# Kernel tuning notes

Hardware: AMD Instinct MI355X
Metric: run time of the kernel (lower is better)

The kernel has to match this reference:

```python
import jax, jax.numpy as jnp
import numpy as np

D = 64
H = 4
HD = D // H
N_MOL, E_MOL = 2048, 32768
N_PROT, E_PROT = 8192, 262144
LN_EPS = 1e-5


def _lin_params(key, d_in, d_out):
    k1, k2 = jax.random.split(key)
    lim = 1.0 / np.sqrt(d_in)
    w = jax.random.uniform(k1, (d_in, d_out), minval=-lim, maxval=lim, dtype=jnp.float32)
    b = jax.random.uniform(k2, (d_out,), minval=-lim, maxval=lim, dtype=jnp.float32)
    return w, b


def setup_inputs() -> dict:
    key = jax.random.key(0)
    ks = jax.random.split(key, 20)
    inp = {
        'x_mol': jax.random.normal(ks[0], (N_MOL, D), dtype=jnp.float32),
        'edge_index_mol': jax.random.randint(ks[1], (2, E_MOL), 0, N_MOL),
        'edge_attr_mol': jax.random.normal(ks[2], (E_MOL, D), dtype=jnp.float32),
        'x_prot': jax.random.normal(ks[3], (N_PROT, D), dtype=jnp.float32),
        'edge_index_prot': jax.random.randint(ks[4], (2, E_PROT), 0, N_PROT),
        'edge_attr_prot': jax.random.normal(ks[5], (E_PROT, D), dtype=jnp.float32),
    }
    # GINE MLPs: Linear -> ReLU -> Linear
    inp['mol_w1'], inp['mol_b1'] = _lin_params(ks[6], D, D)
    inp['mol_w2'], inp['mol_b2'] = _lin_params(ks[7], D, D)
    inp['prot_w1'], inp['prot_b1'] = _lin_params(ks[8], D, D)
    inp['prot_w2'], inp['prot_b2'] = _lin_params(ks[9], D, D)
    # cross-attn mol->prot (query=mol, key/value=prot)
    inp['mp_wq'], inp['mp_bq'] = _lin_params(ks[10], D, D)
    inp['mp_wk'], inp['mp_bk'] = _lin_params(ks[11], D, D)
    inp['mp_wv'], inp['mp_bv'] = _lin_params(ks[12], D, D)
    # cross-attn prot->mol (query=prot, key/value=mol)
    inp['pm_wq'], inp['pm_bq'] = _lin_params(ks[13], D, D)
    inp['pm_wk'], inp['pm_bk'] = _lin_params(ks[14], D, D)
    inp['pm_wv'], inp['pm_bv'] = _lin_params(ks[15], D, D)
    # layer norms
    inp['ln_mol_g'] = jnp.ones((D,), jnp.float32)
    inp['ln_mol_b'] = jnp.zeros((D,), jnp.float32)
    inp['ln_prot_g'] = jnp.ones((D,), jnp.float32)
    inp['ln_prot_b'] = jnp.zeros((D,), jnp.float32)
    return inp


def _gine_conv(x, edge_index, edge_attr, w1, b1, w2, b2, n_nodes):
    # message: relu(x_j + edge_attr); aggregate: mean at target; update: MLP((1+eps)*x + aggr), eps=0
    src, dst = edge_index[0], edge_index[1]
    msg = jax.nn.relu(x[src] + edge_attr)                       # [E, D]
    ssum = jax.ops.segment_sum(msg, dst, num_segments=n_nodes)  # [N, D]
    cnt = jax.ops.segment_sum(jnp.ones((msg.shape[0],), msg.dtype), dst, num_segments=n_nodes)
    aggr = ssum / jnp.maximum(cnt, 1.0)[:, None]
    h = x + aggr
    h = jax.nn.relu(h @ w1 + b1) @ w2 + b2
    return h


def _cross_attn(q_nodes, k_nodes, wq, bq, wk, bk, wv, bv):
    Nq, Nk = q_nodes.shape[0], k_nodes.shape[0]
    Q = (q_nodes @ wq + bq).reshape(Nq, H, HD)
    K = (k_nodes @ wk + bk).reshape(Nk, H, HD)
    V = (k_nodes @ wv + bv).reshape(Nk, H, HD)
    scores = jnp.einsum('qhd,khd->hqk', Q, K) / np.sqrt(HD).astype(np.float32)
    attn = jax.nn.softmax(scores, axis=-1)                      # [H, Nq, Nk]
    out = jnp.einsum('hqk,khd->qhd', attn, V).reshape(Nq, D)
    return out


def _layer_norm(x, g, b):
    mu = jnp.mean(x, axis=-1, keepdims=True)
    var = jnp.mean(jnp.square(x - mu), axis=-1, keepdims=True)
    return (x - mu) * jax.lax.rsqrt(var + LN_EPS) * g + b


def reference(x_mol, edge_index_mol, edge_attr_mol, x_prot, edge_index_prot, edge_attr_prot,
              mol_w1, mol_b1, mol_w2, mol_b2, prot_w1, prot_b1, prot_w2, prot_b2,
              mp_wq, mp_bq, mp_wk, mp_bk, mp_wv, mp_bv,
              pm_wq, pm_bq, pm_wk, pm_bk, pm_wv, pm_bv,
              ln_mol_g, ln_mol_b, ln_prot_g, ln_prot_b):
    h_mol = jax.nn.relu(_gine_conv(x_mol, edge_index_mol, edge_attr_mol,
                                   mol_w1, mol_b1, mol_w2, mol_b2, x_mol.shape[0]))
    h_prot = jax.nn.relu(_gine_conv(x_prot, edge_index_prot, edge_attr_prot,
                                    prot_w1, prot_b1, prot_w2, prot_b2, x_prot.shape[0]))
    h_mol_attn = _cross_attn(h_mol, h_prot, mp_wq, mp_bq, mp_wk, mp_bk, mp_wv, mp_bv)
    h_prot_attn = _cross_attn(h_prot, h_mol, pm_wq, pm_bq, pm_wk, pm_bk, pm_wv, pm_bv)
    out_mol = _layer_norm(h_mol + h_mol_attn, ln_mol_g, ln_mol_b)
    out_prot = _layer_norm(h_prot + h_prot_attn, ln_prot_g, ln_prot_b)
    return out_mol, out_prot
```

## Files before the change

kernel.cpp:

```cpp
#include <hip/hip_runtime.h>

#define NM 2048
#define EM 32768
#define NP 8192
#define EP 262144

typedef __attribute__((ext_vector_type(8))) short short8;
typedef __attribute__((ext_vector_type(4))) float f32x4;

#define LOG2E 1.44269504088896340736f

__device__ __forceinline__ float e2(float x) { return __builtin_amdgcn_exp2f(x); }
__device__ __forceinline__ unsigned int pk_bf16_tr(float a, float b) {
    return __builtin_amdgcn_perm(__float_as_uint(a), __float_as_uint(b), 0x03020706u);
}
__device__ __forceinline__ unsigned short cvt_bf16(float f) {
    unsigned int u = __float_as_uint(f);
    u = (u + 0x7fff + ((u >> 16) & 1)) >> 16;
    return (unsigned short)u;
}

__global__ __launch_bounds__(256) void hist_kernel(
    const int* __restrict__ ei_m, const int* __restrict__ ei_p,
    int* __restrict__ cnt_m, int* __restrict__ cnt_p)
{
    int idx = blockIdx.x * 256 + threadIdx.x;
    if (idx < EM) atomicAdd(&cnt_m[ei_m[EM + idx]], 1);
    int j = idx - EM;
    if (j >= 0 && j < EP) atomicAdd(&cnt_p[ei_p[EP + j]], 1);
}

__global__ __launch_bounds__(256) void scan_kernel(
    const int* __restrict__ cnt_m, const int* __restrict__ cnt_p,
    int* __restrict__ start_m, int* __restrict__ start_p,
    int* __restrict__ cur_m, int* __restrict__ cur_p)
{
    const int* cnt; int* start; int* cur; int n;
    if (blockIdx.x == 0) { cnt = cnt_m; start = start_m; cur = cur_m; n = NM; }
    else                 { cnt = cnt_p; start = start_p; cur = cur_p; n = NP; }
    int per = n >> 8;
    int tid = threadIdx.x;
    int base = tid * per;
    int s = 0;
    for (int i = 0; i < per; i++) s += cnt[base + i];
    __shared__ int wsum[4];
    int lane = tid & 63, w = tid >> 6;
    int v = s;
    #pragma unroll
    for (int off = 1; off < 64; off <<= 1) {
        int u = __shfl_up(v, off, 64);
        if (lane >= off) v += u;
    }
    if (lane == 63) wsum[w] = v;
    __syncthreads();
    int wo = 0;
    for (int i = 0; i < w; i++) wo += wsum[i];
    int run = wo + v - s;
    for (int i = 0; i < per; i++) {
        start[base + i] = run; cur[base + i] = run;
        run += cnt[base + i];
    }
    if (tid == 255) start[n] = run;
}

__global__ __launch_bounds__(256) void scatter_kernel(
    const int* __restrict__ ei_m, const int* __restrict__ ei_p,
    int* __restrict__ cur_m, int* __restrict__ cur_p,
    int* __restrict__ pidx_m, int* __restrict__ pidx_p)
{
    int idx = blockIdx.x * 256 + threadIdx.x;
    if (idx < EM) {
        int d = ei_m[EM + idx];
        int pos = atomicAdd(&cur_m[d], 1);
        pidx_m[pos] = (idx << 11) | ei_m[idx];
    }
    int j = idx - EM;
    if (j >= 0 && j < EP) {
        int d = ei_p[EP + j];
        int pos = atomicAdd(&cur_p[d], 1);
        pidx_p[pos] = (j << 13) | ei_p[j];
    }
}

__global__ __launch_bounds__(256) void node_aggr_kernel(
    const float* __restrict__ x_m, const float* __restrict__ ea_m,
    const int* __restrict__ start_m, const int* __restrict__ pidx_m,
    const float* __restrict__ x_p, const float* __restrict__ ea_p,
    const int* __restrict__ start_p, const int* __restrict__ pidx_p,
    float* __restrict__ h0_m, float* __restrict__ h0_p)
{
    int wave = threadIdx.x >> 6, lane = threadIdx.x & 63;
    int nid = blockIdx.x * 4 + wave;
    const float *x, *ea; const int *start, *pidx; float* h0; int n, sh, msk;
    if (nid < NM) { x = x_m; ea = ea_m; start = start_m; pidx = pidx_m; h0 = h0_m; n = nid; sh = 11; msk = 2047; }
    else          { x = x_p; ea = ea_p; start = start_p; pidx = pidx_p; h0 = h0_p; n = nid - NM; sh = 13; msk = 8191; }
    int b  = __builtin_amdgcn_readfirstlane(start[n]);
    int e  = __builtin_amdgcn_readfirstlane(start[n + 1]);
    int deg = e - b;
    const int* pp = pidx + b;
    float acc = 0.f;
    int j = 0;
    for (; j + 8 <= deg; j += 8) {
        int v0 = __builtin_amdgcn_readfirstlane(pp[j]);
        int v1 = __builtin_amdgcn_readfirstlane(pp[j + 1]);
        int v2 = __builtin_amdgcn_readfirstlane(pp[j + 2]);
        int v3 = __builtin_amdgcn_readfirstlane(pp[j + 3]);
        int v4 = __builtin_amdgcn_readfirstlane(pp[j + 4]);
        int v5 = __builtin_amdgcn_readfirstlane(pp[j + 5]);
        int v6 = __builtin_amdgcn_readfirstlane(pp[j + 6]);
        int v7 = __builtin_amdgcn_readfirstlane(pp[j + 7]);
        float a0 = ea[(size_t)(((unsigned)v0) >> sh) * 64 + lane];
        float a1 = ea[(size_t)(((unsigned)v1) >> sh) * 64 + lane];
        float a2 = ea[(size_t)(((unsigned)v2) >> sh) * 64 + lane];
        float a3 = ea[(size_t)(((unsigned)v3) >> sh) * 64 + lane];
        float a4 = ea[(size_t)(((unsigned)v4) >> sh) * 64 + lane];
        float a5 = ea[(size_t)(((unsigned)v5) >> sh) * 64 + lane];
        float a6 = ea[(size_t)(((unsigned)v6) >> sh) * 64 + lane];
        float a7 = ea[(size_t)(((unsigned)v7) >> sh) * 64 + lane];
        float y0 = x[(size_t)(v0 & msk) * 64 + lane];
        float y1 = x[(size_t)(v1 & msk) * 64 + lane];
        float y2 = x[(size_t)(v2 & msk) * 64 + lane];
        float y3 = x[(size_t)(v3 & msk) * 64 + lane];
        float y4 = x[(size_t)(v4 & msk) * 64 + lane];
        float y5 = x[(size_t)(v5 & msk) * 64 + lane];
        float y6 = x[(size_t)(v6 & msk) * 64 + lane];
        float y7 = x[(size_t)(v7 & msk) * 64 + lane];
        acc += fmaxf(y0 + a0, 0.f); acc += fmaxf(y1 + a1, 0.f);
        acc += fmaxf(y2 + a2, 0.f); acc += fmaxf(y3 + a3, 0.f);
        acc += fmaxf(y4 + a4, 0.f); acc += fmaxf(y5 + a5, 0.f);
        acc += fmaxf(y6 + a6, 0.f); acc += fmaxf(y7 + a7, 0.f);
    }
    for (; j < deg; ++j) {
        int v0 = __builtin_amdgcn_readfirstlane(pp[j]);
        acc += fmaxf(x[(size_t)(v0 & msk) * 64 + lane] + ea[(size_t)(((unsigned)v0) >> sh) * 64 + lane], 0.f);
    }
    float aggr = acc / fmaxf((float)deg, 1.f);
    h0[(size_t)n * 64 + lane] = x[(size_t)n * 64 + lane] + aggr;
}

__global__ __launch_bounds__(256) void gine_mlp_kernel(
    const float* __restrict__ h0_m, const float* __restrict__ h0_p,
    const float* __restrict__ w1m, const float* __restrict__ b1m,
    const float* __restrict__ w2m, const float* __restrict__ b2m,
    const float* __restrict__ w1p, const float* __restrict__ b1p,
    const float* __restrict__ w2p, const float* __restrict__ b2p,
    float* __restrict__ hm, float* __restrict__ hp)
{
    const float *h0, *w1, *b1, *w2, *b2; float* out; int row0;
    if (blockIdx.x < NM / 16) {
        h0 = h0_m; w1 = w1m; b1 = b1m; w2 = w2m; b2 = b2m; out = hm;
        row0 = blockIdx.x * 16;
    } else {
        h0 = h0_p; w1 = w1p; b1 = b1p; w2 = w2p; b2 = b2p; out = hp;
        row0 = (blockIdx.x - NM / 16) * 16;
    }
    __shared__ float sW1[4096], sW2[4096], sb1[64], sb2[64];
    __shared__ float sh0[16][64], sh1[16][64];
    int t = threadIdx.x;
    for (int i = t; i < 4096; i += 256) { sW1[i] = w1[i]; sW2[i] = w2[i]; }
    if (t < 64) { sb1[t] = b1[t]; sb2[t] = b2[t]; }
    for (int i = t; i < 16 * 64; i += 256) {
        int r = i >> 6, c = i & 63;
        sh0[r][c] = h0[(size_t)(row0 + r) * 64 + c];
    }
    __syncthreads();
    int j = t & 63, rs = t >> 6;
    for (int r = rs; r < 16; r += 4) {
        float a = sb1[j];
        #pragma unroll
        for (int c = 0; c < 64; c++) a += sh0[r][c] * sW1[c * 64 + j];
        sh1[r][j] = fmaxf(a, 0.0f);
    }
    __syncthreads();
    for (int r = rs; r < 16; r += 4) {
        float a = sb2[j];
        #pragma unroll
        for (int c = 0; c < 64; c++) a += sh1[r][c] * sW2[c * 64 + j];
        out[(size_t)(row0 + r) * 64 + j] = fmaxf(a, 0.0f);
    }
}

__global__ __launch_bounds__(256) void qkv_bf16_kernel(
    const float* __restrict__ hm, const float* __restrict__ hp,
    const float* __restrict__ wq_m, const float* __restrict__ bq_m,
    const float* __restrict__ wk_m, const float* __restrict__ bk_m,
    const float* __restrict__ wv_m, const float* __restrict__ bv_m,
    const float* __restrict__ wq_p, const float* __restrict__ bq_p,
    const float* __restrict__ wk_p, const float* __restrict__ bk_p,
    const float* __restrict__ wv_p, const float* __restrict__ bv_p,
    unsigned short* __restrict__ Qm, unsigned short* __restrict__ Km, unsigned short* __restrict__ Vtm,
    unsigned short* __restrict__ Qp, unsigned short* __restrict__ Kp, unsigned short* __restrict__ Vtp,
    int* __restrict__ norms)
{
    const float *x, *wq, *bq, *wk, *bk, *wv, *bv;
    unsigned short *Q, *K, *Vt; int row0, N, nbase;
    if (blockIdx.x < NM / 16) {
        x = hm; wq = wq_m; bq = bq_m; wk = wk_m; bk = bk_m; wv = wv_m; bv = bv_m;
        Q = Qm; K = Km; Vt = Vtm; N = NM; row0 = blockIdx.x * 16; nbase = 0;
    } else {
        x = hp; wq = wq_p; bq = bq_p; wk = wk_p; bk = bk_p; wv = wv_p; bv = bv_p;
        Q = Qp; K = Kp; Vt = Vtp; N = NP; row0 = (blockIdx.x - NM / 16) * 16; nbase = 2;
    }
    __shared__ float sWq[4096], sWk[4096], sWv[4096];
    __shared__ float sbq[64], sbk[64], sbv[64];
    __shared__ float sh0[16][64];
    __shared__ float rmx[8];
    int t = threadIdx.x;
    for (int i = t; i < 4096; i += 256) { sWq[i] = wq[i]; sWk[i] = wk[i]; sWv[i] = wv[i]; }
    if (t < 64) { sbq[t] = bq[t]; sbk[t] = bk[t]; sbv[t] = bv[t]; }
    for (int i = t; i < 16 * 64; i += 256) {
        int r = i >> 6, c = i & 63;
        sh0[r][c] = x[(size_t)(row0 + r) * 64 + c];
    }
    __syncthreads();
    int j = t & 63, rs = t >> 6;
    float qmx = 0.f, kmx = 0.f;
    for (int r = rs; r < 16; r += 4) {
        float aq = sbq[j], ak = sbk[j], av = sbv[j];
        #pragma unroll
        for (int c = 0; c < 64; c++) {
            float h = sh0[r][c];
            aq += h * sWq[c * 64 + j];
            ak += h * sWk[c * 64 + j];
            av += h * sWv[c * 64 + j];
        }
        float qs = aq * (0.25f * LOG2E);
        size_t o = (size_t)(row0 + r) * 64 + j;
        Q[o] = cvt_bf16(qs);
        K[o] = cvt_bf16(ak);
        Vt[(size_t)j * N + row0 + r] = cvt_bf16(av);
        float qsq = qs * qs, ksq = ak * ak;
        #pragma unroll
        for (int o2 = 1; o2 <= 8; o2 <<= 1) {
            qsq += __shfl_xor(qsq, o2, 64);
            ksq += __shfl_xor(ksq, o2, 64);
        }
        qmx = fmaxf(qmx, qsq);
        kmx = fmaxf(kmx, ksq);
    }
    qmx = fmaxf(qmx, __shfl_xor(qmx, 16, 64)); qmx = fmaxf(qmx, __shfl_xor(qmx, 32, 64));
    kmx = fmaxf(kmx, __shfl_xor(kmx, 16, 64)); kmx = fmaxf(kmx, __shfl_xor(kmx, 32, 64));
    if (j == 0) { rmx[rs] = qmx; rmx[4 + rs] = kmx; }
    __syncthreads();
    if (t == 0) {
        float q4 = fmaxf(fmaxf(rmx[0], rmx[1]), fmaxf(rmx[2], rmx[3]));
        float k4 = fmaxf(fmaxf(rmx[4], rmx[5]), fmaxf(rmx[6], rmx[7]));
        atomicMax(&norms[nbase],     __float_as_int(sqrtf(q4)));
        atomicMax(&norms[nbase + 1], __float_as_int(sqrtf(k4)));
    }
}

__global__ __launch_bounds__(256) void attn_kernel(
    const unsigned short* __restrict__ Qm, const unsigned short* __restrict__ Km,
    const unsigned short* __restrict__ Vtm,
    const unsigned short* __restrict__ Qp, const unsigned short* __restrict__ Kp,
    const unsigned short* __restrict__ Vtp,
    const int* __restrict__ norms, float* __restrict__ partial)
{
    __shared__ unsigned int plds[4][2][16][20];
    int t = threadIdx.x;
    int wave = t >> 6;
    int lane = t & 63;
    int qrow = lane & 15;
    int quad = lane >> 4;
    int W = blockIdx.x * 4 + wave;

    const unsigned short *Q, *K, *Vt; int Nk; float m;
    int chunk, h, qt2, Tbase, T1off;
    if (W < 2048) {
        Q = Qm; K = Kp; Vt = Vtp; Nk = NP;
        m = __int_as_float(norms[0]) * __int_as_float(norms[3]);
        chunk = W & 7; h = (W >> 3) & 3; qt2 = W >> 5;
        Tbase = W + qt2 * 32; T1off = 32;
    } else {
        int W2 = W - 2048;
        Q = Qp; K = Km; Vt = Vtm; Nk = NM;
        m = __int_as_float(norms[2]) * __int_as_float(norms[1]);
        chunk = W2 & 1; h = (W2 >> 1) & 3; qt2 = W2 >> 3;
        Tbase = 4096 + W2 + qt2 * 8; T1off = 8;
    }

    short8 qfA = {}, qfB = {};
    if (quad < 2) {
        qfA = *(const short8*)(Q + ((size_t)(qt2 * 32 + qrow)) * 64 + h * 16 + quad * 8);
        qfB = *(const short8*)(Q + ((size_t)(qt2 * 32 + 16 + qrow)) * 64 + h * 16 + quad * 8);
    }

    const f32x4 zero4 = {0.f, 0.f, 0.f, 0.f};
    int kbase = chunk * 1024;
    const unsigned short* krow = K + (size_t)(kbase + qrow) * 64 + h * 16 + quad * 8;
    const unsigned short* vrow = Vt + ((size_t)(h * 16 + qrow)) * Nk + kbase + quad * 8;

    float lA = 0.0f, lB = 0.0f;
    f32x4 accA = zero4, accB = zero4;

    short8 kf0p[2], kf1p[2], vfp[2];
    #pragma unroll
    for (int i = 0; i < 2; ++i) {
        kf0p[i] = (short8){}; kf1p[i] = (short8){};
        if (quad < 2) {
            kf0p[i] = *(const short8*)(krow + (size_t)(i * 32) * 64);
            kf1p[i] = *(const short8*)(krow + (size_t)(i * 32 + 16) * 64);
        }
        vfp[i] = *(const short8*)(vrow + i * 32);
    }

    #pragma unroll 2
    for (int it = 0; it < 32; ++it) {
        short8 kf0 = kf0p[it & 1], kf1 = kf1p[it & 1], vf = vfp[it & 1];
        if (it < 30) {
            int off = (it + 2) * 32;
            if (quad < 2) {
                kf0p[it & 1] = *(const short8*)(krow + (size_t)off * 64);
                kf1p[it & 1] = *(const short8*)(krow + (size_t)(off + 16) * 64);
            }
            vfp[it & 1] = *(const short8*)(vrow + off);
        }

        f32x4 s0A = __builtin_amdgcn_mfma_f32_16x16x32_bf16(kf0, qfA, zero4, 0, 0, 0);
        f32x4 s1A = __builtin_amdgcn_mfma_f32_16x16x32_bf16(kf1, qfA, zero4, 0, 0, 0);
        f32x4 s0B = __builtin_amdgcn_mfma_f32_16x16x32_bf16(kf0, qfB, zero4, 0, 0, 0);
        f32x4 s1B = __builtin_amdgcn_mfma_f32_16x16x32_bf16(kf1, qfB, zero4, 0, 0, 0);

        float a00 = e2(s0A.x - m), a01 = e2(s0A.y - m), a02 = e2(s0A.z - m), a03 = e2(s0A.w - m);
        float a10 = e2(s1A.x - m), a11 = e2(s1A.y - m), a12 = e2(s1A.z - m), a13 = e2(s1A.w - m);
        float b00 = e2(s0B.x - m), b01 = e2(s0B.y - m), b02 = e2(s0B.z - m), b03 = e2(s0B.w - m);
        float b10 = e2(s1B.x - m), b11 = e2(s1B.y - m), b12 = e2(s1B.z - m), b13 = e2(s1B.w - m);
        lA += (((a00 + a01) + (a02 + a03)) + ((a10 + a11) + (a12 + a13)));
        lB += (((b00 + b01) + (b02 + b03)) + ((b10 + b11) + (b12 + b13)));

        uint2 wA0; wA0.x = pk_bf16_tr(a00, a01); wA0.y = pk_bf16_tr(a02, a03);
        uint2 wA1; wA1.x = pk_bf16_tr(a10, a11); wA1.y = pk_bf16_tr(a12, a13);
        uint2 wB0; wB0.x = pk_bf16_tr(b00, b01); wB0.y = pk_bf16_tr(b02, b03);
        uint2 wB1; wB1.x = pk_bf16_tr(b10, b11); wB1.y = pk_bf16_tr(b12, b13);
        *(uint2*)&plds[wave][0][qrow][quad * 2] = wA0;
        *(uint2*)&plds[wave][0][qrow][8 + quad * 2] = wA1;
        *(uint2*)&plds[wave][1][qrow][quad * 2] = wB0;
        *(uint2*)&plds[wave][1][qrow][8 + quad * 2] = wB1;
        short8 pfA = *(short8*)&plds[wave][0][qrow][quad * 4];
        short8 pfB = *(short8*)&plds[wave][1][qrow][quad * 4];

        accA = __builtin_amdgcn_mfma_f32_16x16x32_bf16(vf, pfA, accA, 0, 0, 0);
        accB = __builtin_amdgcn_mfma_f32_16x16x32_bf16(vf, pfB, accB, 0, 0, 0);
    }

    float ltA = lA + __shfl_xor(lA, 16, 64); ltA += __shfl_xor(ltA, 32, 64);
    float ltB = lB + __shfl_xor(lB, 16, 64); ltB += __shfl_xor(ltB, 32, 64);

    float* pb0 = partial + (size_t)Tbase * 288;
    *(f32x4*)&pb0[qrow * 16 + quad * 4] = accA;
    if (quad == 0) pb0[272 + qrow] = ltA;
    float* pb1 = partial + (size_t)(Tbase + T1off) * 288;
    *(f32x4*)&pb1[qrow * 16 + quad * 4] = accB;
    if (quad == 0) pb1[272 + qrow] = ltB;
}

__global__ __launch_bounds__(256) void merge_ln_kernel(
    const float* __restrict__ partial,
    const float* __restrict__ h_m, const float* __restrict__ h_p,
    const float* __restrict__ gm, const float* __restrict__ bm,
    const float* __restrict__ gp, const float* __restrict__ bp_,
    float* __restrict__ out)
{
    int t = threadIdx.x;
    int grow = blockIdx.x * 4 + (t >> 6);
    int c = t & 63;
    const float *pbase, *hbuf, *g, *bb; float* o; int NC, row;
    if (grow < NM) { pbase = partial;               hbuf = h_m; g = gm; bb = bm;  o = out;             NC = 8; row = grow; }
    else           { pbase = partial + 4096 * 288;  hbuf = h_p; g = gp; bb = bp_; o = out + NM * 64;   NC = 2; row = grow - NM; }
    int hi = c >> 4, d = c & 15;
    int qt = row >> 4, ql = row & 15;
    const float* base = pbase + (size_t)(qt * 4 + hi) * NC * 288;
    float L = 0.0f, A = 0.0f;
    for (int cc = 0; cc < NC; ++cc) {
        L += base[cc * 288 + 272 + ql];
        A += base[cc * 288 + ql * 16 + d];
    }
    float v = hbuf[(size_t)row * 64 + c] + A / L;
    float s = v;
    #pragma unroll
    for (int o2 = 32; o2 >= 1; o2 >>= 1) s += __shfl_xor(s, o2, 64);
    float mu = s * (1.0f / 64.0f);
    float dv = v - mu;
    float sq = dv * dv;
    #pragma unroll
    for (int o2 = 32; o2 >= 1; o2 >>= 1) sq += __shfl_xor(sq, o2, 64);
    float var = sq * (1.0f / 64.0f);
    o[(size_t)row * 64 + c] = dv * rsqrtf(var + 1e-5f) * g[c] + bb[c];
}

extern "C" void kernel_launch(void* const* d_in, const int* in_sizes, int n_in,
                              void* d_out, int out_size, void* d_ws, size_t ws_size,
                              hipStream_t stream)
{
    const float* x_mol   = (const float*)d_in[0];
    const int*   ei_mol  = (const int*)  d_in[1];
    const float* ea_mol  = (const float*)d_in[2];
    const float* x_prot  = (const float*)d_in[3];
    const int*   ei_prot = (const int*)  d_in[4];
    const float* ea_prot = (const float*)d_in[5];
    const float* mol_w1  = (const float*)d_in[6];
    const float* mol_b1  = (const float*)d_in[7];
    const float* mol_w2  = (const float*)d_in[8];
    const float* mol_b2  = (const float*)d_in[9];
    const float* prot_w1 = (const float*)d_in[10];
    const float* prot_b1 = (const float*)d_in[11];
    const float* prot_w2 = (const float*)d_in[12];
    const float* prot_b2 = (const float*)d_in[13];
    const float* mp_wq = (const float*)d_in[14]; const float* mp_bq = (const float*)d_in[15];
    const float* mp_wk = (const float*)d_in[16]; const float* mp_bk = (const float*)d_in[17];
    const float* mp_wv = (const float*)d_in[18]; const float* mp_bv = (const float*)d_in[19];
    const float* pm_wq = (const float*)d_in[20]; const float* pm_bq = (const float*)d_in[21];
    const float* pm_wk = (const float*)d_in[22]; const float* pm_bk = (const float*)d_in[23];
    const float* pm_wv = (const float*)d_in[24]; const float* pm_bv = (const float*)d_in[25];
    const float* ln_mol_g  = (const float*)d_in[26];
    const float* ln_mol_b  = (const float*)d_in[27];
    const float* ln_prot_g = (const float*)d_in[28];
    const float* ln_prot_b = (const float*)d_in[29];

    float* ws = (float*)d_ws;
    float* h_mol   = ws;
    float* h_prot  = h_mol + 131072;
    float* partial = h_prot + 524288;
    float* h0_mol  = partial;
    float* h0_prot = h0_mol + 131072;
    int* ip      = (int*)(partial + 2359296);
    int* cnt_m   = ip;
    int* cnt_p   = cnt_m + 2048;
    int* norms   = cnt_p + 8192;
    int* start_m = norms + 4;
    int* start_p = start_m + 2052;
    int* cur_m   = start_p + 8196;
    int* cur_p   = cur_m + 2048;
    int* pidx_m  = cur_p + 8192;
    int* pidx_p  = pidx_m + 32768;
    unsigned short* bf = (unsigned short*)(pidx_p + 262144);
    unsigned short* Qm  = bf;
    unsigned short* Km  = Qm + 131072;
    unsigned short* Vtm = Km + 131072;
    unsigned short* Qp  = Vtm + 131072;
    unsigned short* Kp  = Qp + 524288;
    unsigned short* Vtp = Kp + 524288;

    hipMemsetAsync(cnt_m, 0, (size_t)(2048 + 8192 + 4) * sizeof(int), stream);

    const int EB = (EM + EP) / 256;
    hist_kernel<<<EB, 256, 0, stream>>>(ei_mol, ei_prot, cnt_m, cnt_p);
    scan_kernel<<<2, 256, 0, stream>>>(cnt_m, cnt_p, start_m, start_p, cur_m, cur_p);
    scatter_kernel<<<EB, 256, 0, stream>>>(ei_mol, ei_prot, cur_m, cur_p, pidx_m, pidx_p);
    node_aggr_kernel<<<(NM + NP) / 4, 256, 0, stream>>>(
        x_mol, ea_mol, start_m, pidx_m,
        x_prot, ea_prot, start_p, pidx_p, h0_mol, h0_prot);

    gine_mlp_kernel<<<(NM + NP) / 16, 256, 0, stream>>>(
        h0_mol, h0_prot, mol_w1, mol_b1, mol_w2, mol_b2,
        prot_w1, prot_b1, prot_w2, prot_b2, h_mol, h_prot);

    qkv_bf16_kernel<<<(NM + NP) / 16, 256, 0, stream>>>(
        h_mol, h_prot,
        mp_wq, mp_bq, pm_wk, pm_bk, pm_wv, pm_bv,
        pm_wq, pm_bq, mp_wk, mp_bk, mp_wv, mp_bv,
        Qm, Km, Vtm, Qp, Kp, Vtp, norms);

    attn_kernel<<<1024, 256, 0, stream>>>(Qm, Km, Vtm, Qp, Kp, Vtp, norms, partial);

    float* out = (float*)d_out;
    merge_ln_kernel<<<(NM + NP) / 4, 256, 0, stream>>>(
        partial, h_mol, h_prot, ln_mol_g, ln_mol_b, ln_prot_g, ln_prot_b, out);
}
```

Measured before the change: 305.3 us.

## Fuse GINE MLP with QKV projection and software-pipeline attention PV step

```diff
diff --git a/kernel.cpp b/kernel.cpp
--- a/kernel.cpp
+++ b/kernel.cpp
@@ -138,97 +138,77 @@
     h0[(size_t)n * 64 + lane] = x[(size_t)n * 64 + lane] + aggr;
 }
 
-__global__ __launch_bounds__(256) void gine_mlp_kernel(
+__global__ __launch_bounds__(256) void mlp_qkv_kernel(
     const float* __restrict__ h0_m, const float* __restrict__ h0_p,
     const float* __restrict__ w1m, const float* __restrict__ b1m,
     const float* __restrict__ w2m, const float* __restrict__ b2m,
     const float* __restrict__ w1p, const float* __restrict__ b1p,
     const float* __restrict__ w2p, const float* __restrict__ b2p,
-    float* __restrict__ hm, float* __restrict__ hp)
-{
-    const float *h0, *w1, *b1, *w2, *b2; float* out; int row0;
-    if (blockIdx.x < NM / 16) {
-        h0 = h0_m; w1 = w1m; b1 = b1m; w2 = w2m; b2 = b2m; out = hm;
-        row0 = blockIdx.x * 16;
-    } else {
-        h0 = h0_p; w1 = w1p; b1 = b1p; w2 = w2p; b2 = b2p; out = hp;
-        row0 = (blockIdx.x - NM / 16) * 16;
-    }
-    __shared__ float sW1[4096], sW2[4096], sb1[64], sb2[64];
-    __shared__ float sh0[16][64], sh1[16][64];
-    int t = threadIdx.x;
-    for (int i = t; i < 4096; i += 256) { sW1[i] = w1[i]; sW2[i] = w2[i]; }
-    if (t < 64) { sb1[t] = b1[t]; sb2[t] = b2[t]; }
-    for (int i = t; i < 16 * 64; i += 256) {
-        int r = i >> 6, c = i & 63;
-        sh0[r][c] = h0[(size_t)(row0 + r) * 64 + c];
-    }
-    __syncthreads();
-    int j = t & 63, rs = t >> 6;
-    for (int r = rs; r < 16; r += 4) {
-        float a = sb1[j];
-        #pragma unroll
-        for (int c = 0; c < 64; c++) a += sh0[r][c] * sW1[c * 64 + j];
-        sh1[r][j] = fmaxf(a, 0.0f);
-    }
-    __syncthreads();
-    for (int r = rs; r < 16; r += 4) {
-        float a = sb2[j];
-        #pragma unroll
-        for (int c = 0; c < 64; c++) a += sh1[r][c] * sW2[c * 64 + j];
-        out[(size_t)(row0 + r) * 64 + j] = fmaxf(a, 0.0f);
-    }
-}
-
-__global__ __launch_bounds__(256) void qkv_bf16_kernel(
-    const float* __restrict__ hm, const float* __restrict__ hp,
     const float* __restrict__ wq_m, const float* __restrict__ bq_m,
     const float* __restrict__ wk_m, const float* __restrict__ bk_m,
     const float* __restrict__ wv_m, const float* __restrict__ bv_m,
     const float* __restrict__ wq_p, const float* __restrict__ bq_p,
     const float* __restrict__ wk_p, const float* __restrict__ bk_p,
     const float* __restrict__ wv_p, const float* __restrict__ bv_p,
+    float* __restrict__ hm, float* __restrict__ hp,
     unsigned short* __restrict__ Qm, unsigned short* __restrict__ Km, unsigned short* __restrict__ Vtm,
     unsigned short* __restrict__ Qp, unsigned short* __restrict__ Kp, unsigned short* __restrict__ Vtp,
     int* __restrict__ norms)
 {
-    const float *x, *wq, *bq, *wk, *bk, *wv, *bv;
-    unsigned short *Q, *K, *Vt; int row0, N, nbase;
+    const float *h0, *w1, *b1, *w2, *b2, *wq, *bq, *wk, *bk, *wv, *bv;
+    float* hout; unsigned short *Q, *K, *Vt; int row0, N, nbase;
     if (blockIdx.x < NM / 16) {
-        x = hm; wq = wq_m; bq = bq_m; wk = wk_m; bk = bk_m; wv = wv_m; bv = bv_m;
-        Q = Qm; K = Km; Vt = Vtm; N = NM; row0 = blockIdx.x * 16; nbase = 0;
+        h0 = h0_m; w1 = w1m; b1 = b1m; w2 = w2m; b2 = b2m;
+        wq = wq_m; bq = bq_m; wk = wk_m; bk = bk_m; wv = wv_m; bv = bv_m;
+        hout = hm; Q = Qm; K = Km; Vt = Vtm; N = NM; row0 = blockIdx.x * 16; nbase = 0;
     } else {
-        x = hp; wq = wq_p; bq = bq_p; wk = wk_p; bk = bk_p; wv = wv_p; bv = bv_p;
-        Q = Qp; K = Kp; Vt = Vtp; N = NP; row0 = (blockIdx.x - NM / 16) * 16; nbase = 2;
-    }
-    __shared__ float sWq[4096], sWk[4096], sWv[4096];
-    __shared__ float sbq[64], sbk[64], sbv[64];
-    __shared__ float sh0[16][64];
+        h0 = h0_p; w1 = w1p; b1 = b1p; w2 = w2p; b2 = b2p;
+        wq = wq_p; bq = bq_p; wk = wk_p; bk = bk_p; wv = wv_p; bv = bv_p;
+        hout = hp; Q = Qp; K = Kp; Vt = Vtp; N = NP; row0 = (blockIdx.x - NM / 16) * 16; nbase = 2;
+    }
+    __shared__ float sWa[4096], sWb[4096], sWc[4096];
+    __shared__ float sb1[64], sb2[64], sbq[64], sbk[64], sbv[64];
+    __shared__ float sh0[16][64], sh1[16][64];
     __shared__ float rmx[8];
     int t = threadIdx.x;
-    for (int i = t; i < 4096; i += 256) { sWq[i] = wq[i]; sWk[i] = wk[i]; sWv[i] = wv[i]; }
-    if (t < 64) { sbq[t] = bq[t]; sbk[t] = bk[t]; sbv[t] = bv[t]; }
+    for (int i = t; i < 4096; i += 256) { sWa[i] = w1[i]; sWb[i] = w2[i]; sWc[i] = wq[i]; }
+    if (t < 64) { sb1[t] = b1[t]; sb2[t] = b2[t]; sbq[t] = bq[t]; sbk[t] = bk[t]; sbv[t] = bv[t]; }
     for (int i = t; i < 16 * 64; i += 256) {
         int r = i >> 6, c = i & 63;
-        sh0[r][c] = x[(size_t)(row0 + r) * 64 + c];
+        sh0[r][c] = h0[(size_t)(row0 + r) * 64 + c];
     }
     __syncthreads();
     int j = t & 63, rs = t >> 6;
+    for (int r = rs; r < 16; r += 4) {
+        float a = sb1[j];
+        #pragma unroll
+        for (int c = 0; c < 64; c++) a += sh0[r][c] * sWa[c * 64 + j];
+        sh1[r][j] = fmaxf(a, 0.0f);
+    }
+    __syncthreads();
+    for (int r = rs; r < 16; r += 4) {
+        float a = sb2[j];
+        #pragma unroll
+        for (int c = 0; c < 64; c++) a += sh1[r][c] * sWb[c * 64 + j];
+        float hval = fmaxf(a, 0.0f);
+        hout[(size_t)(row0 + r) * 64 + j] = hval;
+        sh0[r][j] = hval;
+    }
+    for (int i = t; i < 4096; i += 256) sWa[i] = wk[i];
+    __syncthreads();
     float qmx = 0.f, kmx = 0.f;
     for (int r = rs; r < 16; r += 4) {
-        float aq = sbq[j], ak = sbk[j], av = sbv[j];
+        float aq = sbq[j], ak = sbk[j];
         #pragma unroll
         for (int c = 0; c < 64; c++) {
             float h = sh0[r][c];
-            aq += h * sWq[c * 64 + j];
-            ak += h * sWk[c * 64 + j];
-            av += h * sWv[c * 64 + j];
+            aq += h * sWc[c * 64 + j];
+            ak += h * sWa[c * 64 + j];
         }
         float qs = aq * (0.25f * LOG2E);
         size_t o = (size_t)(row0 + r) * 64 + j;
         Q[o] = cvt_bf16(qs);
         K[o] = cvt_bf16(ak);
-        Vt[(size_t)j * N + row0 + r] = cvt_bf16(av);
         float qsq = qs * qs, ksq = ak * ak;
         #pragma unroll
         for (int o2 = 1; o2 <= 8; o2 <<= 1) {
@@ -238,10 +218,17 @@
         qmx = fmaxf(qmx, qsq);
         kmx = fmaxf(kmx, ksq);
     }
+    for (int i = t; i < 4096; i += 256) sWb[i] = wv[i];
     qmx = fmaxf(qmx, __shfl_xor(qmx, 16, 64)); qmx = fmaxf(qmx, __shfl_xor(qmx, 32, 64));
     kmx = fmaxf(kmx, __shfl_xor(kmx, 16, 64)); kmx = fmaxf(kmx, __shfl_xor(kmx, 32, 64));
     if (j == 0) { rmx[rs] = qmx; rmx[4 + rs] = kmx; }
     __syncthreads();
+    for (int r = rs; r < 16; r += 4) {
+        float av = sbv[j];
+        #pragma unroll
+        for (int c = 0; c < 64; c++) av += sh0[r][c] * sWb[c * 64 + j];
+        Vt[(size_t)j * N + row0 + r] = cvt_bf16(av);
+    }
     if (t == 0) {
         float q4 = fmaxf(fmaxf(rmx[0], rmx[1]), fmaxf(rmx[2], rmx[3]));
         float k4 = fmaxf(fmaxf(rmx[4], rmx[5]), fmaxf(rmx[6], rmx[7]));
@@ -257,7 +244,7 @@
     const unsigned short* __restrict__ Vtp,
     const int* __restrict__ norms, float* __restrict__ partial)
 {
-    __shared__ unsigned int plds[4][2][16][20];
+    __shared__ unsigned int plds[4][2][2][16][20];
     int t = threadIdx.x;
     int wave = t >> 6;
     int lane = t & 63;
@@ -305,9 +292,41 @@
         vfp[i] = *(const short8*)(vrow + i * 32);
     }
 
-    #pragma unroll 2
-    for (int it = 0; it < 32; ++it) {
+    short8 vf_prev;
+    {
+        short8 kf0 = kf0p[0], kf1 = kf1p[0];
+        vf_prev = vfp[0];
+        {
+            if (quad < 2) {
+                kf0p[0] = *(const short8*)(krow + (size_t)(2 * 32) * 64);
+                kf1p[0] = *(const short8*)(krow + (size_t)(2 * 32 + 16) * 64);
+            }
+            vfp[0] = *(const short8*)(vrow + 2 * 32);
+        }
+        f32x4 s0A = __builtin_amdgcn_mfma_f32_16x16x32_bf16(kf0, qfA, zero4, 0, 0, 0);
+        f32x4 s1A = __builtin_amdgcn_mfma_f32_16x16x32_bf16(kf1, qfA, zero4, 0, 0, 0);
+        f32x4 s0B = __builtin_amdgcn_mfma_f32_16x16x32_bf16(kf0, qfB, zero4, 0, 0, 0);
+        f32x4 s1B = __builtin_amdgcn_mfma_f32_16x16x32_bf16(kf1, qfB, zero4, 0, 0, 0);
+        float a00 = e2(s0A.x - m), a01 = e2(s0A.y - m), a02 = e2(s0A.z - m), a03 = e2(s0A.w - m);
+        float a10 = e2(s1A.x - m), a11 = e2(s1A.y - m), a12 = e2(s1A.z - m), a13 = e2(s1A.w - m);
+        float b00 = e2(s0B.x - m), b01 = e2(s0B.y - m), b02 = e2(s0B.z - m), b03 = e2(s0B.w - m);
+        float b10 = e2(s1B.x - m), b11 = e2(s1B.y - m), b12 = e2(s1B.z - m), b13 = e2(s1B.w - m);
+        lA += (((a00 + a01) + (a02 + a03)) + ((a10 + a11) + (a12 + a13)));
+        lB += (((b00 + b01) + (b02 + b03)) + ((b10 + b11) + (b12 + b13)));
+        uint2 wA0; wA0.x = pk_bf16_tr(a00, a01); wA0.y = pk_bf16_tr(a02, a03);
+        uint2 wA1; wA1.x = pk_bf16_tr(a10, a11); wA1.y = pk_bf16_tr(a12, a13);
+        uint2 wB0; wB0.x = pk_bf16_tr(b00, b01); wB0.y = pk_bf16_tr(b02, b03);
+        uint2 wB1; wB1.x = pk_bf16_tr(b10, b11); wB1.y = pk_bf16_tr(b12, b13);
+        *(uint2*)&plds[wave][0][0][qrow][quad * 2] = wA0;
+        *(uint2*)&plds[wave][0][0][qrow][8 + quad * 2] = wA1;
+        *(uint2*)&plds[wave][1][0][qrow][quad * 2] = wB0;
+        *(uint2*)&plds[wave][1][0][qrow][8 + quad * 2] = wB1;
+    }
+
+    for (int it = 1; it < 32; ++it) {
         short8 kf0 = kf0p[it & 1], kf1 = kf1p[it & 1], vf = vfp[it & 1];
+        short8 pfA = *(short8*)&plds[wave][0][(it - 1) & 1][qrow][quad * 4];
+        short8 pfB = *(short8*)&plds[wave][1][(it - 1) & 1][qrow][quad * 4];
         if (it < 30) {
             int off = (it + 2) * 32;
             if (quad < 2) {
@@ -333,15 +352,20 @@
         uint2 wA1; wA1.x = pk_bf16_tr(a10, a11); wA1.y = pk_bf16_tr(a12, a13);
         uint2 wB0; wB0.x = pk_bf16_tr(b00, b01); wB0.y = pk_bf16_tr(b02, b03);
         uint2 wB1; wB1.x = pk_bf16_tr(b10, b11); wB1.y = pk_bf16_tr(b12, b13);
-        *(uint2*)&plds[wave][0][qrow][quad * 2] = wA0;
-        *(uint2*)&plds[wave][0][qrow][8 + quad * 2] = wA1;
-        *(uint2*)&plds[wave][1][qrow][quad * 2] = wB0;
-        *(uint2*)&plds[wave][1][qrow][8 + quad * 2] = wB1;
-        short8 pfA = *(short8*)&plds[wave][0][qrow][quad * 4];
-        short8 pfB = *(short8*)&plds[wave][1][qrow][quad * 4];
-
-        accA = __builtin_amdgcn_mfma_f32_16x16x32_bf16(vf, pfA, accA, 0, 0, 0);
-        accB = __builtin_amdgcn_mfma_f32_16x16x32_bf16(vf, pfB, accB, 0, 0, 0);
+        *(uint2*)&plds[wave][0][it & 1][qrow][quad * 2] = wA0;
+        *(uint2*)&plds[wave][0][it & 1][qrow][8 + quad * 2] = wA1;
+        *(uint2*)&plds[wave][1][it & 1][qrow][quad * 2] = wB0;
+        *(uint2*)&plds[wave][1][it & 1][qrow][8 + quad * 2] = wB1;
+
+        accA = __builtin_amdgcn_mfma_f32_16x16x32_bf16(vf_prev, pfA, accA, 0, 0, 0);
+        accB = __builtin_amdgcn_mfma_f32_16x16x32_bf16(vf_prev, pfB, accB, 0, 0, 0);
+        vf_prev = vf;
+    }
+    {
+        short8 pfA = *(short8*)&plds[wave][0][1][qrow][quad * 4];
+        short8 pfB = *(short8*)&plds[wave][1][1][qrow][quad * 4];
+        accA = __builtin_amdgcn_mfma_f32_16x16x32_bf16(vf_prev, pfA, accA, 0, 0, 0);
+        accB = __builtin_amdgcn_mfma_f32_16x16x32_bf16(vf_prev, pfB, accB, 0, 0, 0);
     }
 
     float ltA = lA + __shfl_xor(lA, 16, 64); ltA += __shfl_xor(ltA, 32, 64);
@@ -452,15 +476,12 @@
         x_mol, ea_mol, start_m, pidx_m,
         x_prot, ea_prot, start_p, pidx_p, h0_mol, h0_prot);
 
-    gine_mlp_kernel<<<(NM + NP) / 16, 256, 0, stream>>>(
-        h0_mol, h0_prot, mol_w1, mol_b1, mol_w2, mol_b2,
-        prot_w1, prot_b1, prot_w2, prot_b2, h_mol, h_prot);
-
-    qkv_bf16_kernel<<<(NM + NP) / 16, 256, 0, stream>>>(
-        h_mol, h_prot,
+    mlp_qkv_kernel<<<(NM + NP) / 16, 256, 0, stream>>>(
+        h0_mol, h0_prot,
+        mol_w1, mol_b1, mol_w2, mol_b2, prot_w1, prot_b1, prot_w2, prot_b2,
         mp_wq, mp_bq, pm_wk, pm_bk, pm_wv, pm_bv,
         pm_wq, pm_bq, mp_wk, mp_bk, mp_wv, mp_bv,
-        Qm, Km, Vtm, Qp, Kp, Vtp, norms);
+        h_mol, h_prot, Qm, Km, Vtm, Qp, Kp, Vtp, norms);
 
     attn_kernel<<<1024, 256, 0, stream>>>(Qm, Km, Vtm, Qp, Kp, Vtp, norms, partial);
 
```

Measured after the change: 630.4 us. 106% more time.
